# Performance work log

Measured on AMD Instinct MI355X. Metric: run time of the kernel, lower is better.

## Reference

```python
import jax, jax.numpy as jnp
import numpy as np

EMBED = 128
HEADS = 32          # embed_dim // 4, forced by fuse Conv2d channel counts
HEAD_DIM = EMBED // HEADS  # 4
WS = (4, 7, 7)
N = WS[0] * WS[1] * WS[2]  # 196 tokens per window
B = 64              # batch * num_windows
SCALE = HEAD_DIM ** -0.5
EPS = 1e-5


def _rel_index():
    d, h, w = WS
    coords = np.stack(np.meshgrid(np.arange(d), np.arange(h), np.arange(w), indexing='ij'))
    flat = coords.reshape(3, -1)                       # [3, N]
    rel = (flat[:, :, None] - flat[:, None, :]).transpose(1, 2, 0).astype(np.int64)  # [N,N,3]
    rel[:, :, 0] += d - 1
    rel[:, :, 1] += h - 1
    rel[:, :, 2] += w - 1
    rel[:, :, 0] *= (2 * h - 1) * (2 * w - 1)
    rel[:, :, 1] *= (2 * w - 1)
    return rel.sum(-1).astype(np.int32)                # [N, N]


def setup_inputs() -> dict:
    key = jax.random.key(0)
    ks = jax.random.split(key, 7)
    d, h, w = WS
    tbl = (2 * d - 1) * (2 * h - 1) * (2 * w - 1)
    return {
        'x_in':      jax.random.normal(ks[0], (B, N, EMBED), dtype=jnp.float32),
        'x_in2':     jax.random.normal(ks[1], (B, N, EMBED), dtype=jnp.float32),
        'qkv_w':     jax.random.normal(ks[2], (3 * EMBED, EMBED), dtype=jnp.float32) * 0.02,
        'proj_w':    jax.random.normal(ks[3], (EMBED, EMBED), dtype=jnp.float32) * 0.02,
        'proj_b':    jnp.zeros((EMBED,), dtype=jnp.float32),
        'rpb_table': jax.random.normal(ks[4], (tbl, HEADS), dtype=jnp.float32) * 0.02,
        'fuse_w':    jax.random.normal(ks[5], (EMBED // 4, EMBED // 2), dtype=jnp.float32) * 0.1,
        'fuse_b':    jnp.zeros((EMBED // 4,), dtype=jnp.float32),
        'rel_idx':   jnp.asarray(_rel_index()),
    }


def _branch(x, qkv_w):
    b, n, c = x.shape
    qkv = (x @ qkv_w.T).reshape(b, n, 3, HEADS, c // HEADS).transpose(2, 0, 3, 1, 4)
    q, k, v = qkv[0] * SCALE, qkv[1], qkv[2]           # [b, H, n, d]
    attn = jnp.einsum('bhnd,bhmd->bhnm', q, k)         # [b, H, n, n]
    return attn, v


def reference(x_in, x_in2, qkv_w, proj_w, proj_b, rpb_table, fuse_w, fuse_b, rel_idx):
    b, n, c = x_in.shape
    attn1, v1 = _branch(x_in, qkv_w)
    attn2, v2 = _branch(x_in2, qkv_w)

    # conv-gated value fusion: Conv2d 1x1 over channel dim (= 2H) + InstanceNorm2d + ReLU + Sigmoid
    vcat = jnp.concatenate([v1, v2], axis=1)           # [b, 2H, n, d]
    v = jnp.einsum('bcnd,oc->bond', vcat, fuse_w) + fuse_b[None, :, None, None]  # [b, H, n, d]
    mu = v.mean(axis=(2, 3), keepdims=True)
    var = v.var(axis=(2, 3), keepdims=True)            # biased, as InstanceNorm2d
    v = (v - mu) * jax.lax.rsqrt(var + EPS)
    v = jax.nn.sigmoid(jax.nn.relu(v))

    # relative position bias: gather [n*n] rows of table -> [H, n, n]
    bias = rpb_table[rel_idx[:n, :n].reshape(-1)].reshape(n, n, HEADS).transpose(2, 0, 1)

    attn = jax.nn.softmax(attn1 + attn2 + bias[None], axis=-1)  # [b, H, n, n]
    x = jnp.einsum('bhnm,bhmd->bhnd', attn, v).transpose(0, 2, 1, 3).reshape(b, n, c)
    return x @ proj_w.T + proj_b
```

## Files before the change

### kernel.cpp

```cpp
#include <hip/hip_runtime.h>
#include <hip/hip_bf16.h>
#include <stdint.h>

#define NB   64
#define NTOK 196
#define NH   32
#define HD   4
#define CE   128
#define NM   38416

typedef __bf16 bf16x8 __attribute__((ext_vector_type(8)));
typedef float  f32x4  __attribute__((ext_vector_type(4)));

#define QSCALE 0.7213475204444817f
#define LOG2E  1.4426950408889634f

__device__ __forceinline__ float u2f(unsigned short u) {
    union { unsigned int i; float f; } z;
    z.i = ((unsigned int)u) << 16;
    return z.f;
}
__device__ __forceinline__ unsigned short f2u(float f) {
    union { float f; unsigned int i; } z; z.f = f;
    unsigned int x = z.i;
    return (unsigned short)((x + 0x7fffu + ((x >> 16) & 1u)) >> 16);
}

extern "C" __global__ __launch_bounds__(256) void qkv_gemm(
    const float* __restrict__ x1,
    const float* __restrict__ x2,
    const float* __restrict__ qkvw,
    unsigned short* __restrict__ Qb, unsigned short* __restrict__ Kb,
    unsigned short* __restrict__ V)
{
    __shared__ alignas(16) unsigned short AT[64][136];
    __shared__ alignas(16) unsigned short BT[64][136];
    const int tid = threadIdx.x;
    const int r0 = blockIdx.x * 64;
    const int j0 = blockIdx.y * 64;

    for (int idx = tid; idx < 2048; idx += 256) {
        int row = idx >> 5, k0 = (idx & 31) << 2;
        int r = r0 + row;
        const float* xp = (r >= 12544) ? x2 : x1;
        int rem = r - ((r >= 12544) ? 12544 : 0);
        float4 v = *(const float4*)&xp[rem * 128 + k0];
        ushort4 u; u.x = f2u(v.x); u.y = f2u(v.y); u.z = f2u(v.z); u.w = f2u(v.w);
        *(ushort4*)&AT[row][k0] = u;
    }
    for (int idx = tid; idx < 2048; idx += 256) {
        int row = idx >> 5, k0 = (idx & 31) << 2;
        float4 v = *(const float4*)&qkvw[(j0 + row) * 128 + k0];
        ushort4 u; u.x = f2u(v.x); u.y = f2u(v.y); u.z = f2u(v.z); u.w = f2u(v.w);
        *(ushort4*)&BT[row][k0] = u;
    }
    __syncthreads();

    const int lane = tid & 63, w = tid >> 6;
    const int wj = (w >> 1) * 32;
    const int wt = (w & 1) * 32;
    const int quad = lane >> 4, tc = lane & 15;

    f32x4 acc[2][2] = {};
#pragma unroll
    for (int ks = 0; ks < 4; ++ks) {
        int k0 = ks * 32 + quad * 8;
        bf16x8 a0 = *(const bf16x8*)&BT[wj + tc][k0];
        bf16x8 a1 = *(const bf16x8*)&BT[wj + 16 + tc][k0];
        bf16x8 b0 = *(const bf16x8*)&AT[wt + tc][k0];
        bf16x8 b1 = *(const bf16x8*)&AT[wt + 16 + tc][k0];
        acc[0][0] = __builtin_amdgcn_mfma_f32_16x16x32_bf16(a0, b0, acc[0][0], 0, 0, 0);
        acc[0][1] = __builtin_amdgcn_mfma_f32_16x16x32_bf16(a0, b1, acc[0][1], 0, 0, 0);
        acc[1][0] = __builtin_amdgcn_mfma_f32_16x16x32_bf16(a1, b0, acc[1][0], 0, 0, 0);
        acc[1][1] = __builtin_amdgcn_mfma_f32_16x16x32_bf16(a1, b1, acc[1][1], 0, 0, 0);
    }

    const int sel = j0 >> 7;
#pragma unroll
    for (int mi = 0; mi < 2; ++mi) {
        int jbase = (j0 + wj + mi * 16 + quad * 4) & 127;
        int hh = jbase >> 2;
#pragma unroll
        for (int ni = 0; ni < 2; ++ni) {
            int tok = r0 + wt + ni * 16 + tc;
            int branch = (tok >= 12544) ? 1 : 0;
            int rem = tok - branch * 12544;
            int bb = rem / 196;
            int nn = rem - bb * 196;
            union { uint2 v; unsigned short s[4]; } pk2;
            if (sel == 0) {
#pragma unroll
                for (int r = 0; r < 4; ++r) pk2.s[r] = f2u(acc[mi][ni][r] * QSCALE);
                *(uint2*)&Qb[((bb * 32 + hh) * 196 + nn) * 8 + branch * 4] = pk2.v;
            } else if (sel == 1) {
#pragma unroll
                for (int r = 0; r < 4; ++r) pk2.s[r] = f2u(acc[mi][ni][r]);
                *(uint2*)&Kb[((bb * 32 + hh) * 196 + nn) * 8 + branch * 4] = pk2.v;
            } else {
#pragma unroll
                for (int r = 0; r < 4; ++r) pk2.s[r] = f2u(acc[mi][ni][r]);
                *(uint2*)&V[(bb * 64 + branch * 32 + hh) * 784 + nn * 4] = pk2.v;
            }
        }
    }
}

extern "C" __global__ __launch_bounds__(256) void bias_build(
    const int* __restrict__ rel_idx, const float* __restrict__ rpb,
    unsigned short* __restrict__ biasM)
{
    const int qt = blockIdx.x;
    const int h  = blockIdx.y;
    const int tid = threadIdx.x, lane = tid & 63, wv = tid >> 6;
    const int quad = lane >> 4, tc = lane & 15;
    for (int nt = wv; nt < 14; nt += 4) {
        union { uint2 v; unsigned short s[4]; } e;
#pragma unroll
        for (int r = 0; r < 4; ++r) {
            int q   = qt * 16 + tc;
            int key = nt * 16 + quad * 4 + r;
            unsigned short u = 0xFF80;
            if (q < 196 && key < 196) {
                int idx = rel_idx[q * 196 + key];
                u = f2u(rpb[idx * 32 + h] * LOG2E);
            }
            e.s[r] = u;
        }
        *(uint2*)(biasM + (((h * 13 + qt) * 14 + nt) * 64 + lane) * 4) = e.v;
    }
}

__device__ __forceinline__ float block_sum(float v, float* red, int tid) {
#pragma unroll
    for (int off = 32; off > 0; off >>= 1) v += __shfl_down(v, off);
    __syncthreads();
    if ((tid & 63) == 0) red[tid >> 6] = v;
    __syncthreads();
    return red[0] + red[1] + red[2] + red[3];
}

__device__ __forceinline__ float act_sig_relu(float x) {
    return x > 0.f ? __fdividef(1.f, 1.f + __expf(-x)) : 0.5f;
}

extern "C" __global__ __launch_bounds__(256) void fuse_kernel(
    const unsigned short* __restrict__ V,
    const float* __restrict__ fuse_w,
    const float* __restrict__ fuse_b,
    float* __restrict__ Vf)
{
    const int b = blockIdx.x, o0 = blockIdx.y * 2;
    const int tid = threadIdx.x;
    __shared__ float fws[2][64];
    __shared__ float red[4];
    if (tid < 128) fws[tid >> 6][tid & 63] = fuse_w[(o0 + (tid >> 6)) * 64 + (tid & 63)];
    __syncthreads();

    const unsigned short* Vb = V + b * 64 * 784;
    float a0[3] = {0.f, 0.f, 0.f}, a1[3] = {0.f, 0.f, 0.f};
    float t0 = 0.f, t1 = 0.f;
    const bool tail = tid < 16;
    for (int c = 0; c < 64; ++c) {
        float w0 = fws[0][c], w1 = fws[1][c];
        const unsigned short* Vc = Vb + c * 784;
#pragma unroll
        for (int k = 0; k < 3; ++k) {
            float x = u2f(Vc[tid + 256 * k]);
            a0[k] = fmaf(w0, x, a0[k]);
            a1[k] = fmaf(w1, x, a1[k]);
        }
        if (tail) {
            float x = u2f(Vc[tid + 768]);
            t0 = fmaf(w0, x, t0);
            t1 = fmaf(w1, x, t1);
        }
    }
    float fb0 = fuse_b[o0], fb1 = fuse_b[o0 + 1];
#pragma unroll
    for (int k = 0; k < 3; ++k) { a0[k] += fb0; a1[k] += fb1; }
    t0 += fb0; t1 += fb1;

    float s0 = a0[0] + a0[1] + a0[2] + (tail ? t0 : 0.f);
    float q0 = a0[0]*a0[0] + a0[1]*a0[1] + a0[2]*a0[2] + (tail ? t0*t0 : 0.f);
    float s1 = a1[0] + a1[1] + a1[2] + (tail ? t1 : 0.f);
    float q1 = a1[0]*a1[0] + a1[1]*a1[1] + a1[2]*a1[2] + (tail ? t1*t1 : 0.f);

    float S0 = block_sum(s0, red, tid);
    float Q0 = block_sum(q0, red, tid);
    float S1 = block_sum(s1, red, tid);
    float Q1 = block_sum(q1, red, tid);

    const float inv = 1.0f / 784.0f;
    float mu0 = S0 * inv, mu1 = S1 * inv;
    float rs0 = rsqrtf(Q0 * inv - mu0 * mu0 + 1e-5f);
    float rs1 = rsqrtf(Q1 * inv - mu1 * mu1 + 1e-5f);

    float* out0 = Vf + (b * 32 + o0) * 784;
    float* out1 = out0 + 784;
#pragma unroll
    for (int k = 0; k < 3; ++k) {
        int e = tid + 256 * k;
        out0[e] = act_sig_relu((a0[k] - mu0) * rs0);
        out1[e] = act_sig_relu((a1[k] - mu1) * rs1);
    }
    if (tail) {
        out0[tid + 768] = act_sig_relu((t0 - mu0) * rs0);
        out1[tid + 768] = act_sig_relu((t1 - mu1) * rs1);
    }
}

extern "C" __global__ __launch_bounds__(256) void attn_kernel(
    const unsigned short* __restrict__ Qb, const unsigned short* __restrict__ Kb,
    const float* __restrict__ Vf, const unsigned short* __restrict__ biasM,
    unsigned short* __restrict__ Ob)
{
    const int bh = blockIdx.x;
    const int b = bh >> 5, h = bh & 31;
    __shared__ alignas(16) unsigned short Qs[208][8];
    __shared__ alignas(16) unsigned short Ks[224][8];
    __shared__ alignas(16) unsigned short VT[16][232];
    const int tid = threadIdx.x;

    const unsigned short* Qrow = Qb + bh * 196 * 8;
    const unsigned short* Krow = Kb + bh * 196 * 8;
    if (tid < 208) {
        uint4 z = {0, 0, 0, 0};
        uint4 v = (tid < 196) ? *(const uint4*)(Qrow + tid * 8) : z;
        *(uint4*)&Qs[tid][0] = v;
    }
    if (tid < 224) {
        uint4 z = {0, 0, 0, 0};
        uint4 v = (tid < 196) ? *(const uint4*)(Krow + tid * 8) : z;
        *(uint4*)&Ks[tid][0] = v;
    }
    {
        unsigned int* vtw = (unsigned int*)&VT[0][0];
        for (int i = tid; i < (16 * 232) / 2; i += 256) vtw[i] = 0u;
    }
    __syncthreads();
    if (tid < 196) {
        float4 vv = *(const float4*)(Vf + bh * 784 + tid * 4);
        VT[0][tid] = f2u(vv.x); VT[1][tid] = f2u(vv.y);
        VT[2][tid] = f2u(vv.z); VT[3][tid] = f2u(vv.w);
        VT[4][tid] = 0x3F80;
    }
    __syncthreads();

    const int lane = tid & 63, wv = tid >> 6;
    const int quad = lane >> 4, tc = lane & 15;

    bf16x8 vfr[7];
#pragma unroll
    for (int kt = 0; kt < 7; ++kt)
        vfr[kt] = *(const bf16x8*)&VT[tc][kt * 32 + quad * 8];

    const int srcA = ((quad & 1) * 32 + tc) * 4;
    const int srcB = srcA + 64;
    const bool useT1 = quad >= 2;

    const unsigned short* bias_hq0 = biasM + (h * 13) * 3584;

    for (int qt = wv; qt < 13; qt += 4) {
        bf16x8 bq = {};
        if (quad == 0) bq = *(const bf16x8*)&Qs[qt * 16 + tc][0];
        const unsigned short* bq_bias = bias_hq0 + qt * 3584;
        f32x4 Oacc = {};
#pragma unroll
        for (int kt = 0; kt < 7; ++kt) {
            uint2 bw0 = *(const uint2*)(bq_bias + (kt * 2 + 0) * 256 + lane * 4);
            uint2 bw1 = *(const uint2*)(bq_bias + (kt * 2 + 1) * 256 + lane * 4);
            f32x4 s0, s1;
            {
                union { unsigned int u; float f; } c;
                c.u = bw0.x << 16;        s0[0] = c.f;
                c.u = bw0.x & 0xffff0000u; s0[1] = c.f;
                c.u = bw0.y << 16;        s0[2] = c.f;
                c.u = bw0.y & 0xffff0000u; s0[3] = c.f;
                c.u = bw1.x << 16;        s1[0] = c.f;
                c.u = bw1.x & 0xffff0000u; s1[1] = c.f;
                c.u = bw1.y << 16;        s1[2] = c.f;
                c.u = bw1.y & 0xffff0000u; s1[3] = c.f;
            }
            bf16x8 a0 = *(const bf16x8*)&Ks[(kt * 2 + 0) * 16 + tc][0];
            bf16x8 a1 = *(const bf16x8*)&Ks[(kt * 2 + 1) * 16 + tc][0];
            s0 = __builtin_amdgcn_mfma_f32_16x16x32_bf16(a0, bq, s0, 0, 0, 0);
            s1 = __builtin_amdgcn_mfma_f32_16x16x32_bf16(a1, bq, s1, 0, 0, 0);
            union { unsigned int u; __bf16 hh[2]; } t0d0, t0d1, t1d0, t1d1;
            t0d0.hh[0] = (__bf16)exp2f(s0[0]); t0d0.hh[1] = (__bf16)exp2f(s0[1]);
            t0d1.hh[0] = (__bf16)exp2f(s0[2]); t0d1.hh[1] = (__bf16)exp2f(s0[3]);
            t1d0.hh[0] = (__bf16)exp2f(s1[0]); t1d0.hh[1] = (__bf16)exp2f(s1[1]);
            t1d1.hh[0] = (__bf16)exp2f(s1[2]); t1d1.hh[1] = (__bf16)exp2f(s1[3]);
            int p0a = __builtin_amdgcn_ds_bpermute(srcA, (int)t0d0.u);
            int p0b = __builtin_amdgcn_ds_bpermute(srcA, (int)t1d0.u);
            int p1a = __builtin_amdgcn_ds_bpermute(srcA, (int)t0d1.u);
            int p1b = __builtin_amdgcn_ds_bpermute(srcA, (int)t1d1.u);
            int p2a = __builtin_amdgcn_ds_bpermute(srcB, (int)t0d0.u);
            int p2b = __builtin_amdgcn_ds_bpermute(srcB, (int)t1d0.u);
            int p3a = __builtin_amdgcn_ds_bpermute(srcB, (int)t0d1.u);
            int p3b = __builtin_amdgcn_ds_bpermute(srcB, (int)t1d1.u);
            union { int d[4]; bf16x8 v; } pf;
            pf.d[0] = useT1 ? p0b : p0a;
            pf.d[1] = useT1 ? p1b : p1a;
            pf.d[2] = useT1 ? p2b : p2a;
            pf.d[3] = useT1 ? p3b : p3a;
            Oacc = __builtin_amdgcn_mfma_f32_16x16x32_bf16(vfr[kt], pf.v, Oacc, 0, 0, 0);
        }
        float rs = __shfl(Oacc[0], 16 + tc);
        int q = qt * 16 + tc;
        if (quad == 0 && q < 196) {
            float inv = __builtin_amdgcn_rcpf(rs);
            union { uint2 v; unsigned short s[4]; } pk2;
            pk2.s[0] = f2u(Oacc[0] * inv);
            pk2.s[1] = f2u(Oacc[1] * inv);
            pk2.s[2] = f2u(Oacc[2] * inv);
            pk2.s[3] = f2u(Oacc[3] * inv);
            *(uint2*)&Ob[(b * 196 + q) * 128 + h * 4] = pk2.v;
        }
    }
}

extern "C" __global__ __launch_bounds__(256) void proj_kernel(
    const unsigned short* __restrict__ Ob, const float* __restrict__ projw,
    const float* __restrict__ projb, float* __restrict__ out)
{
    __shared__ alignas(16) unsigned short AT[64][136];
    __shared__ alignas(16) unsigned short BT[64][136];
    const int tid = threadIdx.x;
    const int r0 = blockIdx.x * 64;
    const int j0 = blockIdx.y * 64;

    for (int idx = tid; idx < 1024; idx += 256) {
        int row = idx >> 4, k0 = (idx & 15) << 3;
        *(uint4*)&AT[row][k0] = *(const uint4*)&Ob[(r0 + row) * 128 + k0];
    }
    for (int idx = tid; idx < 2048; idx += 256) {
        int row = idx >> 5, k0 = (idx & 31) << 2;
        float4 v = *(const float4*)&projw[(j0 + row) * 128 + k0];
        ushort4 u; u.x = f2u(v.x); u.y = f2u(v.y); u.z = f2u(v.z); u.w = f2u(v.w);
        *(ushort4*)&BT[row][k0] = u;
    }
    __syncthreads();

    const int lane = tid & 63, w = tid >> 6;
    const int wm = (w >> 1) * 32, wn = (w & 1) * 32;
    const int quad = lane >> 4, tcol = lane & 15;

    f32x4 acc[2][2] = {};
#pragma unroll
    for (int ks = 0; ks < 4; ++ks) {
        int k0 = ks * 32 + quad * 8;
        bf16x8 a0 = *(const bf16x8*)&AT[wm + tcol][k0];
        bf16x8 a1 = *(const bf16x8*)&AT[wm + 16 + tcol][k0];
        bf16x8 b0 = *(const bf16x8*)&BT[wn + tcol][k0];
        bf16x8 b1 = *(const bf16x8*)&BT[wn + 16 + tcol][k0];
        acc[0][0] = __builtin_amdgcn_mfma_f32_16x16x32_bf16(a0, b0, acc[0][0], 0, 0, 0);
        acc[0][1] = __builtin_amdgcn_mfma_f32_16x16x32_bf16(a0, b1, acc[0][1], 0, 0, 0);
        acc[1][0] = __builtin_amdgcn_mfma_f32_16x16x32_bf16(a1, b0, acc[1][0], 0, 0, 0);
        acc[1][1] = __builtin_amdgcn_mfma_f32_16x16x32_bf16(a1, b1, acc[1][1], 0, 0, 0);
    }

#pragma unroll
    for (int mi = 0; mi < 2; ++mi) {
#pragma unroll
        for (int ni = 0; ni < 2; ++ni) {
            int j = j0 + wn + ni * 16 + tcol;
            float pb = projb[j];
#pragma unroll
            for (int reg = 0; reg < 4; ++reg) {
                int r = r0 + wm + mi * 16 + quad * 4 + reg;
                out[r * 128 + j] = acc[mi][ni][reg] + pb;
            }
        }
    }
}

extern "C" void kernel_launch(void* const* d_in, const int* in_sizes, int n_in,
                              void* d_out, int out_size, void* d_ws, size_t ws_size,
                              hipStream_t stream)
{
    const float* x1    = (const float*)d_in[0];
    const float* x2    = (const float*)d_in[1];
    const float* qkvw  = (const float*)d_in[2];
    const float* projw = (const float*)d_in[3];
    const float* projb = (const float*)d_in[4];
    const float* rpb   = (const float*)d_in[5];
    const float* fw    = (const float*)d_in[6];
    const float* fb    = (const float*)d_in[7];
    const int*   rel   = (const int*)d_in[8];
    float* out = (float*)d_out;

    char* w = (char*)d_ws;
    unsigned short* Qb  = (unsigned short*)(w);
    unsigned short* Kb  = (unsigned short*)(w + 6422528);
    unsigned short* V   = (unsigned short*)(w + 12845056);
    float*          Vf  = (float*)(w + 19267584);
    unsigned short* bM  = (unsigned short*)(w + 25690112);
    unsigned short* Ob  = (unsigned short*)(w + 28672000);

    qkv_gemm  <<<dim3(392, 6), dim3(256), 0, stream>>>(x1, x2, qkvw, Qb, Kb, V);
    bias_build<<<dim3(13, 32), dim3(256), 0, stream>>>(rel, rpb, bM);
    fuse_kernel<<<dim3(64, 16), dim3(256), 0, stream>>>(V, fw, fb, Vf);
    attn_kernel<<<dim3(2048),   dim3(256), 0, stream>>>(Qb, Kb, Vf, bM, Ob);
    proj_kernel<<<dim3(196, 2), dim3(256), 0, stream>>>(Ob, projw, projb, out);
}
```

Measured before the change: 174.0 us.

## Fuse bias build into QKV GEMM and drop bpermute via 16x16x16 MFMA

New measurement: 153.7 us. 11.7% less time.

```diff
diff --git a/kernel.cpp b/kernel.cpp
--- a/kernel.cpp
+++ b/kernel.cpp
@@ -10,6 +10,7 @@
 #define NM   38416
 
 typedef __bf16 bf16x8 __attribute__((ext_vector_type(8)));
+typedef short  bf16x4s __attribute__((ext_vector_type(4)));
 typedef float  f32x4  __attribute__((ext_vector_type(4)));
 
 #define QSCALE 0.7213475204444817f
@@ -26,16 +27,44 @@
     return (unsigned short)((x + 0x7fffu + ((x >> 16) & 1u)) >> 16);
 }
 
-extern "C" __global__ __launch_bounds__(256) void qkv_gemm(
+extern "C" __global__ __launch_bounds__(256) void qkv_bias(
     const float* __restrict__ x1,
     const float* __restrict__ x2,
     const float* __restrict__ qkvw,
+    const int* __restrict__ rel_idx, const float* __restrict__ rpb,
     unsigned short* __restrict__ Qb, unsigned short* __restrict__ Kb,
-    unsigned short* __restrict__ V)
+    unsigned short* __restrict__ V, unsigned short* __restrict__ biasM)
 {
     __shared__ alignas(16) unsigned short AT[64][136];
     __shared__ alignas(16) unsigned short BT[64][136];
     const int tid = threadIdx.x;
+
+    if (blockIdx.y == 6) {
+        const int bx = blockIdx.x;
+        const int qt = bx % 13, h = bx / 13;
+        const int lane = tid & 63, wv = tid >> 6;
+        const int quad = lane >> 4, tc = lane & 15;
+        for (int nt = wv; nt < 14; nt += 4) {
+            union { uint2 v; unsigned short s[4]; } e;
+#pragma unroll
+            for (int r = 0; r < 4; ++r) {
+                int q   = qt * 16 + tc;
+                int key = nt * 16 + quad * 4 + r;
+                unsigned short u = 0xFF80;
+                if (q < 196 && key < 196) {
+                    int idx = rel_idx[q * 196 + key];
+                    u = f2u(rpb[idx * 32 + h] * LOG2E);
+                }
+                e.s[r] = u;
+            }
+            unsigned int off = (((h * 13 + qt) * 7 + (nt >> 1)) * 64 + lane) * 8
+                               + (nt & 1) * 4;
+            *(uint2*)(biasM + off) = e.v;
+        }
+        return;
+    }
+    if (blockIdx.x >= 392) return;
+
     const int r0 = blockIdx.x * 64;
     const int j0 = blockIdx.y * 64;
 
@@ -102,31 +131,6 @@
                 *(uint2*)&V[(bb * 64 + branch * 32 + hh) * 784 + nn * 4] = pk2.v;
             }
         }
-    }
-}
-
-extern "C" __global__ __launch_bounds__(256) void bias_build(
-    const int* __restrict__ rel_idx, const float* __restrict__ rpb,
-    unsigned short* __restrict__ biasM)
-{
-    const int qt = blockIdx.x;
-    const int h  = blockIdx.y;
-    const int tid = threadIdx.x, lane = tid & 63, wv = tid >> 6;
-    const int quad = lane >> 4, tc = lane & 15;
-    for (int nt = wv; nt < 14; nt += 4) {
-        union { uint2 v; unsigned short s[4]; } e;
-#pragma unroll
-        for (int r = 0; r < 4; ++r) {
-            int q   = qt * 16 + tc;
-            int key = nt * 16 + quad * 4 + r;
-            unsigned short u = 0xFF80;
-            if (q < 196 && key < 196) {
-                int idx = rel_idx[q * 196 + key];
-                u = f2u(rpb[idx * 32 + h] * LOG2E);
-            }
-            e.s[r] = u;
-        }
-        *(uint2*)(biasM + (((h * 13 + qt) * 14 + nt) * 64 + lane) * 4) = e.v;
     }
 }
 
@@ -249,61 +253,52 @@
     const int lane = tid & 63, wv = tid >> 6;
     const int quad = lane >> 4, tc = lane & 15;
 
-    bf16x8 vfr[7];
-#pragma unroll
-    for (int kt = 0; kt < 7; ++kt)
-        vfr[kt] = *(const bf16x8*)&VT[tc][kt * 32 + quad * 8];
-
-    const int srcA = ((quad & 1) * 32 + tc) * 4;
-    const int srcB = srcA + 64;
-    const bool useT1 = quad >= 2;
-
-    const unsigned short* bias_hq0 = biasM + (h * 13) * 3584;
+    bf16x4s vfr16[14];
+#pragma unroll
+    for (int t = 0; t < 14; ++t)
+        vfr16[t] = *(const bf16x4s*)&VT[tc][t * 16 + quad * 4];
+
+    const unsigned short* bias_h = biasM + (unsigned)(h * 13) * 3584;
 
     for (int qt = wv; qt < 13; qt += 4) {
         bf16x8 bq = {};
         if (quad == 0) bq = *(const bf16x8*)&Qs[qt * 16 + tc][0];
-        const unsigned short* bq_bias = bias_hq0 + qt * 3584;
+        const unsigned short* bias_q = bias_h + qt * 3584;
         f32x4 Oacc = {};
 #pragma unroll
         for (int kt = 0; kt < 7; ++kt) {
-            uint2 bw0 = *(const uint2*)(bq_bias + (kt * 2 + 0) * 256 + lane * 4);
-            uint2 bw1 = *(const uint2*)(bq_bias + (kt * 2 + 1) * 256 + lane * 4);
+            uint4 bw = *(const uint4*)(bias_q + kt * 512 + lane * 8);
             f32x4 s0, s1;
             {
                 union { unsigned int u; float f; } c;
-                c.u = bw0.x << 16;        s0[0] = c.f;
-                c.u = bw0.x & 0xffff0000u; s0[1] = c.f;
-                c.u = bw0.y << 16;        s0[2] = c.f;
-                c.u = bw0.y & 0xffff0000u; s0[3] = c.f;
-                c.u = bw1.x << 16;        s1[0] = c.f;
-                c.u = bw1.x & 0xffff0000u; s1[1] = c.f;
-                c.u = bw1.y << 16;        s1[2] = c.f;
-                c.u = bw1.y & 0xffff0000u; s1[3] = c.f;
+                c.u = bw.x << 16;          s0[0] = c.f;
+                c.u = bw.x & 0xffff0000u;  s0[1] = c.f;
+                c.u = bw.y << 16;          s0[2] = c.f;
+                c.u = bw.y & 0xffff0000u;  s0[3] = c.f;
+                c.u = bw.z << 16;          s1[0] = c.f;
+                c.u = bw.z & 0xffff0000u;  s1[1] = c.f;
+                c.u = bw.w << 16;          s1[2] = c.f;
+                c.u = bw.w & 0xffff0000u;  s1[3] = c.f;
             }
             bf16x8 a0 = *(const bf16x8*)&Ks[(kt * 2 + 0) * 16 + tc][0];
             bf16x8 a1 = *(const bf16x8*)&Ks[(kt * 2 + 1) * 16 + tc][0];
             s0 = __builtin_amdgcn_mfma_f32_16x16x32_bf16(a0, bq, s0, 0, 0, 0);
             s1 = __builtin_amdgcn_mfma_f32_16x16x32_bf16(a1, bq, s1, 0, 0, 0);
-            union { unsigned int u; __bf16 hh[2]; } t0d0, t0d1, t1d0, t1d1;
-            t0d0.hh[0] = (__bf16)exp2f(s0[0]); t0d0.hh[1] = (__bf16)exp2f(s0[1]);
-            t0d1.hh[0] = (__bf16)exp2f(s0[2]); t0d1.hh[1] = (__bf16)exp2f(s0[3]);
-            t1d0.hh[0] = (__bf16)exp2f(s1[0]); t1d0.hh[1] = (__bf16)exp2f(s1[1]);
-            t1d1.hh[0] = (__bf16)exp2f(s1[2]); t1d1.hh[1] = (__bf16)exp2f(s1[3]);
-            int p0a = __builtin_amdgcn_ds_bpermute(srcA, (int)t0d0.u);
-            int p0b = __builtin_amdgcn_ds_bpermute(srcA, (int)t1d0.u);
-            int p1a = __builtin_amdgcn_ds_bpermute(srcA, (int)t0d1.u);
-            int p1b = __builtin_amdgcn_ds_bpermute(srcA, (int)t1d1.u);
-            int p2a = __builtin_amdgcn_ds_bpermute(srcB, (int)t0d0.u);
-            int p2b = __builtin_amdgcn_ds_bpermute(srcB, (int)t1d0.u);
-            int p3a = __builtin_amdgcn_ds_bpermute(srcB, (int)t0d1.u);
-            int p3b = __builtin_amdgcn_ds_bpermute(srcB, (int)t1d1.u);
-            union { int d[4]; bf16x8 v; } pf;
-            pf.d[0] = useT1 ? p0b : p0a;
-            pf.d[1] = useT1 ? p1b : p1a;
-            pf.d[2] = useT1 ? p2b : p2a;
-            pf.d[3] = useT1 ? p3b : p3a;
-            Oacc = __builtin_amdgcn_mfma_f32_16x16x32_bf16(vfr[kt], pf.v, Oacc, 0, 0, 0);
+            float e0 = __builtin_amdgcn_exp2f(s0[0]);
+            float e1 = __builtin_amdgcn_exp2f(s0[1]);
+            float e2 = __builtin_amdgcn_exp2f(s0[2]);
+            float e3 = __builtin_amdgcn_exp2f(s0[3]);
+            float g0 = __builtin_amdgcn_exp2f(s1[0]);
+            float g1 = __builtin_amdgcn_exp2f(s1[1]);
+            float g2 = __builtin_amdgcn_exp2f(s1[2]);
+            float g3 = __builtin_amdgcn_exp2f(s1[3]);
+            union { int d[2]; bf16x4s v; } pf0, pf1;
+            pf0.d[0] = (int)__builtin_amdgcn_perm(__float_as_uint(e1), __float_as_uint(e0), 0x07060302u);
+            pf0.d[1] = (int)__builtin_amdgcn_perm(__float_as_uint(e3), __float_as_uint(e2), 0x07060302u);
+            pf1.d[0] = (int)__builtin_amdgcn_perm(__float_as_uint(g1), __float_as_uint(g0), 0x07060302u);
+            pf1.d[1] = (int)__builtin_amdgcn_perm(__float_as_uint(g3), __float_as_uint(g2), 0x07060302u);
+            Oacc = __builtin_amdgcn_mfma_f32_16x16x16bf16_1k(vfr16[kt * 2 + 0], pf0.v, Oacc, 0, 0, 0);
+            Oacc = __builtin_amdgcn_mfma_f32_16x16x16bf16_1k(vfr16[kt * 2 + 1], pf1.v, Oacc, 0, 0, 0);
         }
         float rs = __shfl(Oacc[0], 16 + tc);
         int q = qt * 16 + tc;
@@ -397,8 +392,8 @@
     unsigned short* bM  = (unsigned short*)(w + 25690112);
     unsigned short* Ob  = (unsigned short*)(w + 28672000);
 
-    qkv_gemm  <<<dim3(392, 6), dim3(256), 0, stream>>>(x1, x2, qkvw, Qb, Kb, V);
-    bias_build<<<dim3(13, 32), dim3(256), 0, stream>>>(rel, rpb, bM);
+    qkv_bias  <<<dim3(416, 7), dim3(256), 0, stream>>>(x1, x2, qkvw, rel, rpb,
+                                                       Qb, Kb, V, bM);
     fuse_kernel<<<dim3(64, 16), dim3(256), 0, stream>>>(V, fw, fb, Vf);
     attn_kernel<<<dim3(2048),   dim3(256), 0, stream>>>(Qb, Kb, Vf, bM, Ob);
     proj_kernel<<<dim3(196, 2), dim3(256), 0, stream>>>(Ob, projw, projb, out);
```
